# Performance work log

Measured on AMD Instinct MI355X. Metric: run time of the kernel, lower is better.

Reference implementation:

```python
import jax, jax.numpy as jnp
import numpy as np

B, S, DEC, ENC = 64, 4096, 512, 256


def setup_inputs() -> dict:
    key = jax.random.key(0)
    ks = jax.random.split(key, 8)
    scale_d = 1.0 / np.sqrt(DEC)
    scale_e = 1.0 / np.sqrt(ENC)
    return {
        "decoder_hidden": jax.random.normal(ks[0], (B, 1, DEC), jnp.float32),
        "encoder_outputs": jax.random.normal(ks[1], (B, S, ENC), jnp.float32),
        "mask": jax.random.randint(ks[2], (B, S), 0, 2, jnp.int32),
        "Wd": jax.random.normal(ks[3], (DEC, ENC), jnp.float32) * scale_d,
        "bd": jnp.zeros((ENC,), jnp.float32),
        "We": jax.random.normal(ks[4], (ENC, ENC), jnp.float32) * scale_e,
        "be": jnp.zeros((ENC,), jnp.float32),
        "Wa": jax.random.normal(ks[5], (ENC,), jnp.float32) * scale_e,
        "ba": jnp.zeros((1,), jnp.float32),
    }


def reference(decoder_hidden, encoder_outputs, mask, Wd, bd, We, be, Wa, ba):
    # decoder_proj: [B,1,ENC]; encoder_proj: [B,S,ENC]
    decoder_proj = jnp.einsum("bqd,de->bqe", decoder_hidden, Wd) + bd
    encoder_proj = jnp.einsum("bse,ef->bsf", encoder_outputs, We) + be
    energy = jnp.tanh(decoder_proj + encoder_proj)          # [B,S,ENC]
    scores = jnp.einsum("bse,e->bs", energy, Wa) + ba[0]     # [B,S]
    scores = jnp.where(mask == 0, jnp.float32(-1e10), scores)
    attn = jax.nn.softmax(scores, axis=1)                    # [B,S]
    context = jnp.einsum("bs,bse->be", attn, encoder_outputs)[:, None, :]  # [B,1,ENC]
    return context, attn
```

## Files before the change

### kernel.cpp

```cpp
#include <hip/hip_runtime.h>

#define BATCH 64
#define SEQ   4096
#define DECD  512
#define ENC   256
#define TS    128
#define NCHUNK (SEQ / TS)
#define OUT_ATTN (BATCH * ENC)

typedef short  short8  __attribute__((ext_vector_type(8)));
typedef float  floatx4 __attribute__((ext_vector_type(4)));

__device__ __forceinline__ short f2bf(float f) {
    union { float f; unsigned u; } v; v.f = f;
    unsigned u = v.u;
    u += 0x7FFFu + ((u >> 16) & 1u);
    return (short)(u >> 16);
}

__device__ __forceinline__ float bf2f(short s) {
    union { unsigned u; float f; } v;
    v.u = ((unsigned)(unsigned short)s) << 16;
    return v.f;
}

__device__ __forceinline__ float fast_tanh(float x) {
    x = fminf(fmaxf(x, -9.0f), 9.0f);
    float e2 = __expf(2.0f * x);
    float r  = __builtin_amdgcn_rcpf(e2 + 1.0f);
    return fmaf(-2.0f, r, 1.0f);
}

__device__ __forceinline__ void gload_lds16(const short* g, short* l) {
    __builtin_amdgcn_global_load_lds(
        (const __attribute__((address_space(1))) unsigned int*)g,
        (__attribute__((address_space(3))) unsigned int*)l,
        16, 0, 0);
}

__global__ void prep_kernel(const float* __restrict__ dh,
                            const float* __restrict__ Wd,
                            const float* __restrict__ bd,
                            const float* __restrict__ be,
                            const float* __restrict__ We,
                            float* __restrict__ dpb4,
                            short* __restrict__ WeF) {
    __shared__ float dhs[128];
    int blk = blockIdx.x;
    int t = threadIdx.x;
    if (blk < 256) {
        int b = blk >> 2, j = blk & 3;
        if (t < 128) dhs[t] = dh[b * DECD + j * 128 + t];
        __syncthreads();
        const float* wp = Wd + (size_t)(j * 128) * ENC + t;
        float a0 = 0.f, a1 = 0.f, a2 = 0.f, a3 = 0.f;
#pragma unroll 4
        for (int d = 0; d < 128; d += 4) {
            a0 = fmaf(dhs[d],     wp[(size_t)(d)     * ENC], a0);
            a1 = fmaf(dhs[d + 1], wp[(size_t)(d + 1) * ENC], a1);
            a2 = fmaf(dhs[d + 2], wp[(size_t)(d + 2) * ENC], a2);
            a3 = fmaf(dhs[d + 3], wp[(size_t)(d + 3) * ENC], a3);
        }
        float r = (a0 + a1) + (a2 + a3);
        if (j == 0) r += bd[t] + be[t];
        dpb4[(size_t)(b * 4 + j) * ENC + t] = r;
    } else {
        int gid  = (blk - 256) * 256 + t;
        int lane = gid & 63;
        int nt   = (gid >> 6) & 15;
        int kt   = gid >> 10;
        int quad = lane >> 4, l16 = lane & 15;
        int n = nt * 16 + l16;
        short8 v;
#pragma unroll
        for (int j = 0; j < 8; ++j) {
            int k = kt * 32 + quad * 8 + j;
            v[j] = f2bf(We[k * ENC + n]);
        }
        *(short8*)(WeF + gid * 8) = v;
    }
}

__global__ __launch_bounds__(512, 4) void main_kernel(
    const float* __restrict__ enc, const int* __restrict__ mask,
    const short* __restrict__ WeF, const float* __restrict__ dpb4,
    const float* __restrict__ Wa, const float* __restrict__ ba,
    float* __restrict__ out, float* __restrict__ ctx_ws, float* __restrict__ ml_ws)
{
    __shared__ short Bs[32768];
    float* F    = (float*)Bs;
    float* scF  = F;
    float* wgtF = F + 128;
    float* dpbF = F + 256;
    float* waF  = F + 512;
    float* ctxF = F + 768;

    int blk   = blockIdx.x;
    int b     = blk >> 5;
    int chunk = blk & 31;
    int s_base = chunk * TS;
    int t    = threadIdx.x;
    int w    = t >> 6, lane = t & 63;
    int quad = lane >> 4, l16 = lane & 15;

    const float* encB = enc + (size_t)b * SEQ * ENC;
    int row = s_base + w * 16 + l16;
    const float* aRow = encB + (size_t)row * ENC + quad * 8;

    short8 af[8];
#pragma unroll
    for (int kkt = 0; kkt < 4; ++kkt) {
        floatx4 q0 = *(const floatx4*)(aRow + kkt * 32);
        floatx4 q1 = *(const floatx4*)(aRow + kkt * 32 + 4);
        short8 a;
#pragma unroll
        for (int j = 0; j < 4; ++j) { a[j] = f2bf(q0[j]); a[j + 4] = f2bf(q1[j]); }
        af[kkt] = a;
    }

#pragma unroll
    for (int j = 0; j < 8; ++j) {
        int c = j * 8 + w;
        gload_lds16(WeF + c * 512 + lane * 8, Bs + c * 512 + lane * 8);
    }

#pragma unroll
    for (int kkt = 4; kkt < 8; ++kkt) {
        floatx4 q0 = *(const floatx4*)(aRow + kkt * 32);
        floatx4 q1 = *(const floatx4*)(aRow + kkt * 32 + 4);
        short8 a;
#pragma unroll
        for (int j = 0; j < 4; ++j) { a[j] = f2bf(q0[j]); a[j + 4] = f2bf(q1[j]); }
        af[kkt] = a;
    }

    floatx4 acc[16];
#pragma unroll
    for (int nt = 0; nt < 16; ++nt) acc[nt] = (floatx4){0.f, 0.f, 0.f, 0.f};

    __syncthreads();

#pragma unroll
    for (int kkt = 0; kkt < 4; ++kkt) {
        const short* bp = Bs + kkt * 8192 + lane * 8;
#pragma unroll
        for (int ng = 0; ng < 4; ++ng) {
            short8 bf0 = *(const short8*)(bp + (ng * 4 + 0) * 512);
            short8 bf1 = *(const short8*)(bp + (ng * 4 + 1) * 512);
            short8 bf2 = *(const short8*)(bp + (ng * 4 + 2) * 512);
            short8 bf3 = *(const short8*)(bp + (ng * 4 + 3) * 512);
            acc[ng * 4 + 0] = __builtin_amdgcn_mfma_f32_16x16x32_bf16(af[kkt], bf0, acc[ng * 4 + 0], 0, 0, 0);
            acc[ng * 4 + 1] = __builtin_amdgcn_mfma_f32_16x16x32_bf16(af[kkt], bf1, acc[ng * 4 + 1], 0, 0, 0);
            acc[ng * 4 + 2] = __builtin_amdgcn_mfma_f32_16x16x32_bf16(af[kkt], bf2, acc[ng * 4 + 2], 0, 0, 0);
            acc[ng * 4 + 3] = __builtin_amdgcn_mfma_f32_16x16x32_bf16(af[kkt], bf3, acc[ng * 4 + 3], 0, 0, 0);
        }
    }

    __syncthreads();
#pragma unroll
    for (int j = 0; j < 8; ++j) {
        int c = j * 8 + w;
        gload_lds16(WeF + 32768 + c * 512 + lane * 8, Bs + c * 512 + lane * 8);
    }
    __syncthreads();

#pragma unroll
    for (int kkt = 4; kkt < 8; ++kkt) {
        const short* bp = Bs + (kkt - 4) * 8192 + lane * 8;
#pragma unroll
        for (int ng = 0; ng < 4; ++ng) {
            short8 bf0 = *(const short8*)(bp + (ng * 4 + 0) * 512);
            short8 bf1 = *(const short8*)(bp + (ng * 4 + 1) * 512);
            short8 bf2 = *(const short8*)(bp + (ng * 4 + 2) * 512);
            short8 bf3 = *(const short8*)(bp + (ng * 4 + 3) * 512);
            acc[ng * 4 + 0] = __builtin_amdgcn_mfma_f32_16x16x32_bf16(af[kkt], bf0, acc[ng * 4 + 0], 0, 0, 0);
            acc[ng * 4 + 1] = __builtin_amdgcn_mfma_f32_16x16x32_bf16(af[kkt], bf1, acc[ng * 4 + 1], 0, 0, 0);
            acc[ng * 4 + 2] = __builtin_amdgcn_mfma_f32_16x16x32_bf16(af[kkt], bf2, acc[ng * 4 + 2], 0, 0, 0);
            acc[ng * 4 + 3] = __builtin_amdgcn_mfma_f32_16x16x32_bf16(af[kkt], bf3, acc[ng * 4 + 3], 0, 0, 0);
        }
    }

    __syncthreads();
    if (t < 256) {
        const float* dp = dpb4 + (size_t)b * 4 * ENC;
        dpbF[t] = dp[t] + dp[ENC + t] + dp[2 * ENC + t] + dp[3 * ENC + t];
    } else {
        waF[t - 256] = Wa[t - 256];
    }
    __syncthreads();

    float ba0 = ba[0];
    float part[4] = {0.f, 0.f, 0.f, 0.f};
#pragma unroll
    for (int nt = 0; nt < 16; ++nt) {
        int n = nt * 16 + l16;
        float wa  = waF[n];
        float dpv = dpbF[n];
#pragma unroll
        for (int r = 0; r < 4; ++r)
            part[r] = fmaf(wa, fast_tanh(acc[nt][r] + dpv), part[r]);
    }
#pragma unroll
    for (int r = 0; r < 4; ++r) {
        float v = part[r];
        v += __shfl_xor(v, 1);
        v += __shfl_xor(v, 2);
        v += __shfl_xor(v, 4);
        v += __shfl_xor(v, 8);
        part[r] = v;
    }
    if (l16 == 0) {
        int idx0 = w * 16 + quad * 4;
        int s0 = s_base + idx0;
        const int4 mv = *(const int4*)(mask + b * SEQ + s0);
        int mvals[4] = {mv.x, mv.y, mv.z, mv.w};
#pragma unroll
        for (int r = 0; r < 4; ++r) {
            float scv = part[r] + ba0;
            if (mvals[r] == 0) scv = -1e10f;
            scF[idx0 + r] = scv;
            out[OUT_ATTN + (size_t)b * SEQ + s0 + r] = scv;
        }
    }
    __syncthreads();

    float v0 = scF[lane], v1 = scF[lane + 64];
    float m = fmaxf(v0, v1);
    m = fmaxf(m, __shfl_xor(m, 1));
    m = fmaxf(m, __shfl_xor(m, 2));
    m = fmaxf(m, __shfl_xor(m, 4));
    m = fmaxf(m, __shfl_xor(m, 8));
    m = fmaxf(m, __shfl_xor(m, 16));
    m = fmaxf(m, __shfl_xor(m, 32));
    float e0 = __expf(v0 - m), e1 = __expf(v1 - m);
    float l = e0 + e1;
    l += __shfl_xor(l, 1);
    l += __shfl_xor(l, 2);
    l += __shfl_xor(l, 4);
    l += __shfl_xor(l, 8);
    l += __shfl_xor(l, 16);
    l += __shfl_xor(l, 32);
    if (t < TS) wgtF[t] = __expf(scF[t] - m);
    __syncthreads();

    float wrow = wgtF[w * 16 + l16];
#pragma unroll
    for (int kkt = 0; kkt < 8; ++kkt) {
        float c[8];
#pragma unroll
        for (int j = 0; j < 8; ++j)
            c[j] = wrow * bf2f(af[kkt][j]);
#pragma unroll
        for (int j = 0; j < 8; ++j) {
            c[j] += __shfl_xor(c[j], 1);
            c[j] += __shfl_xor(c[j], 2);
            c[j] += __shfl_xor(c[j], 4);
            c[j] += __shfl_xor(c[j], 8);
        }
        if (l16 == 0) {
            floatx4 u0 = {c[0], c[1], c[2], c[3]};
            floatx4 u1 = {c[4], c[5], c[6], c[7]};
            *(floatx4*)(ctxF + w * 256 + kkt * 32 + quad * 8)     = u0;
            *(floatx4*)(ctxF + w * 256 + kkt * 32 + quad * 8 + 4) = u1;
        }
    }
    __syncthreads();

    int cidx = b * NCHUNK + chunk;
    if (t < 256) {
        float cx = 0.f;
#pragma unroll
        for (int w2 = 0; w2 < 8; ++w2) cx += ctxF[w2 * 256 + t];
        ctx_ws[(size_t)cidx * ENC + t] = cx;
    }
    if (t == 0) {
        ml_ws[cidx * 2]     = m;
        ml_ws[cidx * 2 + 1] = l;
    }
}

__global__ void final_kernel(const float* __restrict__ ctx_ws,
                             const float* __restrict__ ml_ws,
                             float* __restrict__ out) {
    int blk = blockIdx.x, b = blk >> 3, j = blk & 7;
    int t = threadIdx.x;
    float m = -3.4e38f;
    for (int c = 0; c < NCHUNK; ++c)
        m = fmaxf(m, ml_ws[(b * NCHUNK + c) * 2]);
    float L = 0.f;
    for (int c = 0; c < NCHUNK; ++c)
        L += ml_ws[(b * NCHUNK + c) * 2 + 1] * __expf(ml_ws[(b * NCHUNK + c) * 2] - m);
    float inv = 1.0f / L;

    if (j == 0) {
        float cx = 0.f;
        for (int c = 0; c < NCHUNK; ++c) {
            float sc_c = __expf(ml_ws[(b * NCHUNK + c) * 2] - m);
            cx += sc_c * ctx_ws[(size_t)(b * NCHUNK + c) * ENC + t];
        }
        out[b * ENC + t] = cx * inv;
    }

    size_t base = OUT_ATTN + (size_t)b * SEQ + j * 512;
    float r0 = out[base + t];
    float r1 = out[base + 256 + t];
    out[base + t]       = __expf(r0 - m) * inv;
    out[base + 256 + t] = __expf(r1 - m) * inv;
}

extern "C" void kernel_launch(void* const* d_in, const int* in_sizes, int n_in,
                              void* d_out, int out_size, void* d_ws, size_t ws_size,
                              hipStream_t stream) {
    const float* dh   = (const float*)d_in[0];
    const float* enc  = (const float*)d_in[1];
    const int*   mask = (const int*)d_in[2];
    const float* Wd   = (const float*)d_in[3];
    const float* bd   = (const float*)d_in[4];
    const float* We   = (const float*)d_in[5];
    const float* be   = (const float*)d_in[6];
    const float* Wa   = (const float*)d_in[7];
    const float* ba   = (const float*)d_in[8];
    float* out = (float*)d_out;

    float* w      = (float*)d_ws;
    float* ctx_ws = w;
    float* ml_ws  = w + BATCH * NCHUNK * ENC;
    float* dpb4   = ml_ws + BATCH * NCHUNK * 2;
    short* WeF    = (short*)(dpb4 + BATCH * 4 * ENC);

    hipLaunchKernelGGL(prep_kernel,  dim3(256 + 32),       dim3(256), 0, stream,
                       dh, Wd, bd, be, We, dpb4, WeF);
    hipLaunchKernelGGL(main_kernel,  dim3(BATCH * NCHUNK), dim3(512), 0, stream,
                       enc, mask, WeF, dpb4, Wa, ba, out, ctx_ws, ml_ws);
    hipLaunchKernelGGL(final_kernel, dim3(BATCH * 8),      dim3(256), 0, stream,
                       ctx_ws, ml_ws, out);
}
```

Before: 491.7 us.

## Make main kernel persistent over eight chunks with We resident in LDS

```diff
diff --git a/kernel.cpp b/kernel.cpp
--- a/kernel.cpp
+++ b/kernel.cpp
@@ -6,6 +6,7 @@
 #define ENC   256
 #define TS    128
 #define NCHUNK (SEQ / TS)
+#define ITERS 8
 #define OUT_ATTN (BATCH * ENC)
 
 typedef short  short8  __attribute__((ext_vector_type(8)));
@@ -81,201 +82,184 @@
     }
 }
 
-__global__ __launch_bounds__(512, 4) void main_kernel(
+__global__ __launch_bounds__(512, 2) void main_kernel(
     const float* __restrict__ enc, const int* __restrict__ mask,
     const short* __restrict__ WeF, const float* __restrict__ dpb4,
     const float* __restrict__ Wa, const float* __restrict__ ba,
     float* __restrict__ out, float* __restrict__ ctx_ws, float* __restrict__ ml_ws)
 {
-    __shared__ short Bs[32768];
-    float* F    = (float*)Bs;
-    float* scF  = F;
-    float* wgtF = F + 128;
-    float* dpbF = F + 256;
-    float* waF  = F + 512;
-    float* ctxF = F + 768;
-
-    int blk   = blockIdx.x;
-    int b     = blk >> 5;
-    int chunk = blk & 31;
-    int s_base = chunk * TS;
+    __shared__ short Bs[65536];
+    __shared__ float scF[TS];
+    __shared__ float wgtF[TS];
+    __shared__ float dpbF[ENC];
+    __shared__ float waF[ENC];
+    __shared__ float ctxF[8 * ENC];
+
+    int blk    = blockIdx.x;
+    int b      = blk >> 2;
+    int chunk0 = (blk & 3) * ITERS;
     int t    = threadIdx.x;
     int w    = t >> 6, lane = t & 63;
     int quad = lane >> 4, l16 = lane & 15;
 
-    const float* encB = enc + (size_t)b * SEQ * ENC;
-    int row = s_base + w * 16 + l16;
-    const float* aRow = encB + (size_t)row * ENC + quad * 8;
-
-    short8 af[8];
-#pragma unroll
-    for (int kkt = 0; kkt < 4; ++kkt) {
-        floatx4 q0 = *(const floatx4*)(aRow + kkt * 32);
-        floatx4 q1 = *(const floatx4*)(aRow + kkt * 32 + 4);
-        short8 a;
-#pragma unroll
-        for (int j = 0; j < 4; ++j) { a[j] = f2bf(q0[j]); a[j + 4] = f2bf(q1[j]); }
-        af[kkt] = a;
-    }
-
-#pragma unroll
-    for (int j = 0; j < 8; ++j) {
-        int c = j * 8 + w;
-        gload_lds16(WeF + c * 512 + lane * 8, Bs + c * 512 + lane * 8);
-    }
-
-#pragma unroll
-    for (int kkt = 4; kkt < 8; ++kkt) {
-        floatx4 q0 = *(const floatx4*)(aRow + kkt * 32);
-        floatx4 q1 = *(const floatx4*)(aRow + kkt * 32 + 4);
-        short8 a;
-#pragma unroll
-        for (int j = 0; j < 4; ++j) { a[j] = f2bf(q0[j]); a[j + 4] = f2bf(q1[j]); }
-        af[kkt] = a;
-    }
-
-    floatx4 acc[16];
-#pragma unroll
-    for (int nt = 0; nt < 16; ++nt) acc[nt] = (floatx4){0.f, 0.f, 0.f, 0.f};
-
-    __syncthreads();
-
-#pragma unroll
-    for (int kkt = 0; kkt < 4; ++kkt) {
-        const short* bp = Bs + kkt * 8192 + lane * 8;
-#pragma unroll
-        for (int ng = 0; ng < 4; ++ng) {
-            short8 bf0 = *(const short8*)(bp + (ng * 4 + 0) * 512);
-            short8 bf1 = *(const short8*)(bp + (ng * 4 + 1) * 512);
-            short8 bf2 = *(const short8*)(bp + (ng * 4 + 2) * 512);
-            short8 bf3 = *(const short8*)(bp + (ng * 4 + 3) * 512);
-            acc[ng * 4 + 0] = __builtin_amdgcn_mfma_f32_16x16x32_bf16(af[kkt], bf0, acc[ng * 4 + 0], 0, 0, 0);
-            acc[ng * 4 + 1] = __builtin_amdgcn_mfma_f32_16x16x32_bf16(af[kkt], bf1, acc[ng * 4 + 1], 0, 0, 0);
-            acc[ng * 4 + 2] = __builtin_amdgcn_mfma_f32_16x16x32_bf16(af[kkt], bf2, acc[ng * 4 + 2], 0, 0, 0);
-            acc[ng * 4 + 3] = __builtin_amdgcn_mfma_f32_16x16x32_bf16(af[kkt], bf3, acc[ng * 4 + 3], 0, 0, 0);
-        }
-    }
-
-    __syncthreads();
-#pragma unroll
-    for (int j = 0; j < 8; ++j) {
-        int c = j * 8 + w;
-        gload_lds16(WeF + 32768 + c * 512 + lane * 8, Bs + c * 512 + lane * 8);
-    }
-    __syncthreads();
-
-#pragma unroll
-    for (int kkt = 4; kkt < 8; ++kkt) {
-        const short* bp = Bs + (kkt - 4) * 8192 + lane * 8;
-#pragma unroll
-        for (int ng = 0; ng < 4; ++ng) {
-            short8 bf0 = *(const short8*)(bp + (ng * 4 + 0) * 512);
-            short8 bf1 = *(const short8*)(bp + (ng * 4 + 1) * 512);
-            short8 bf2 = *(const short8*)(bp + (ng * 4 + 2) * 512);
-            short8 bf3 = *(const short8*)(bp + (ng * 4 + 3) * 512);
-            acc[ng * 4 + 0] = __builtin_amdgcn_mfma_f32_16x16x32_bf16(af[kkt], bf0, acc[ng * 4 + 0], 0, 0, 0);
-            acc[ng * 4 + 1] = __builtin_amdgcn_mfma_f32_16x16x32_bf16(af[kkt], bf1, acc[ng * 4 + 1], 0, 0, 0);
-            acc[ng * 4 + 2] = __builtin_amdgcn_mfma_f32_16x16x32_bf16(af[kkt], bf2, acc[ng * 4 + 2], 0, 0, 0);
-            acc[ng * 4 + 3] = __builtin_amdgcn_mfma_f32_16x16x32_bf16(af[kkt], bf3, acc[ng * 4 + 3], 0, 0, 0);
-        }
-    }
-
-    __syncthreads();
+    const float* encB  = enc + (size_t)b * SEQ * ENC;
+    const float* aRow0 = encB + (size_t)(chunk0 * TS + w * 16 + l16) * ENC + quad * 8;
+
+#pragma unroll
+    for (int j = 0; j < 16; ++j) {
+        int off = j * 4096 + w * 512 + lane * 8;
+        gload_lds16(WeF + off, Bs + off);
+    }
+
     if (t < 256) {
         const float* dp = dpb4 + (size_t)b * 4 * ENC;
         dpbF[t] = dp[t] + dp[ENC + t] + dp[2 * ENC + t] + dp[3 * ENC + t];
     } else {
         waF[t - 256] = Wa[t - 256];
     }
+    float ba0 = ba[0];
+
+    floatx4 pf[16];
+#pragma unroll
+    for (int q = 0; q < 8; ++q) {
+        pf[2 * q]     = *(const floatx4*)(aRow0 + q * 32);
+        pf[2 * q + 1] = *(const floatx4*)(aRow0 + q * 32 + 4);
+    }
+
     __syncthreads();
 
-    float ba0 = ba[0];
-    float part[4] = {0.f, 0.f, 0.f, 0.f};
-#pragma unroll
-    for (int nt = 0; nt < 16; ++nt) {
-        int n = nt * 16 + l16;
-        float wa  = waF[n];
-        float dpv = dpbF[n];
-#pragma unroll
-        for (int r = 0; r < 4; ++r)
-            part[r] = fmaf(wa, fast_tanh(acc[nt][r] + dpv), part[r]);
-    }
-#pragma unroll
-    for (int r = 0; r < 4; ++r) {
-        float v = part[r];
-        v += __shfl_xor(v, 1);
-        v += __shfl_xor(v, 2);
-        v += __shfl_xor(v, 4);
-        v += __shfl_xor(v, 8);
-        part[r] = v;
-    }
-    if (l16 == 0) {
-        int idx0 = w * 16 + quad * 4;
-        int s0 = s_base + idx0;
-        const int4 mv = *(const int4*)(mask + b * SEQ + s0);
-        int mvals[4] = {mv.x, mv.y, mv.z, mv.w};
+    for (int it = 0; it < ITERS; ++it) {
+        int chunk  = chunk0 + it;
+        int s_base = chunk * TS;
+
+        short8 af[8];
+#pragma unroll
+        for (int kkt = 0; kkt < 8; ++kkt) {
+            short8 a;
+#pragma unroll
+            for (int j = 0; j < 4; ++j) {
+                a[j]     = f2bf(pf[2 * kkt][j]);
+                a[j + 4] = f2bf(pf[2 * kkt + 1][j]);
+            }
+            af[kkt] = a;
+        }
+
+        if (it + 1 < ITERS) {
+            const float* aN = aRow0 + (size_t)(it + 1) * TS * ENC;
+#pragma unroll
+            for (int q = 0; q < 8; ++q) {
+                pf[2 * q]     = *(const floatx4*)(aN + q * 32);
+                pf[2 * q + 1] = *(const floatx4*)(aN + q * 32 + 4);
+            }
+        }
+
+        floatx4 acc[16];
+#pragma unroll
+        for (int nt = 0; nt < 16; ++nt) acc[nt] = (floatx4){0.f, 0.f, 0.f, 0.f};
+
+#pragma unroll
+        for (int kkt = 0; kkt < 8; ++kkt) {
+            const short* bp = Bs + kkt * 8192 + lane * 8;
+#pragma unroll
+            for (int ng = 0; ng < 4; ++ng) {
+                short8 bf0 = *(const short8*)(bp + (ng * 4 + 0) * 512);
+                short8 bf1 = *(const short8*)(bp + (ng * 4 + 1) * 512);
+                short8 bf2 = *(const short8*)(bp + (ng * 4 + 2) * 512);
+                short8 bf3 = *(const short8*)(bp + (ng * 4 + 3) * 512);
+                acc[ng * 4 + 0] = __builtin_amdgcn_mfma_f32_16x16x32_bf16(af[kkt], bf0, acc[ng * 4 + 0], 0, 0, 0);
+                acc[ng * 4 + 1] = __builtin_amdgcn_mfma_f32_16x16x32_bf16(af[kkt], bf1, acc[ng * 4 + 1], 0, 0, 0);
+                acc[ng * 4 + 2] = __builtin_amdgcn_mfma_f32_16x16x32_bf16(af[kkt], bf2, acc[ng * 4 + 2], 0, 0, 0);
+                acc[ng * 4 + 3] = __builtin_amdgcn_mfma_f32_16x16x32_bf16(af[kkt], bf3, acc[ng * 4 + 3], 0, 0, 0);
+            }
+        }
+
+        float part[4] = {0.f, 0.f, 0.f, 0.f};
+#pragma unroll
+        for (int nt = 0; nt < 16; ++nt) {
+            int n = nt * 16 + l16;
+            float wa  = waF[n];
+            float dpv = dpbF[n];
+#pragma unroll
+            for (int r = 0; r < 4; ++r)
+                part[r] = fmaf(wa, fast_tanh(acc[nt][r] + dpv), part[r]);
+        }
 #pragma unroll
         for (int r = 0; r < 4; ++r) {
-            float scv = part[r] + ba0;
-            if (mvals[r] == 0) scv = -1e10f;
-            scF[idx0 + r] = scv;
-            out[OUT_ATTN + (size_t)b * SEQ + s0 + r] = scv;
-        }
-    }
-    __syncthreads();
-
-    float v0 = scF[lane], v1 = scF[lane + 64];
-    float m = fmaxf(v0, v1);
-    m = fmaxf(m, __shfl_xor(m, 1));
-    m = fmaxf(m, __shfl_xor(m, 2));
-    m = fmaxf(m, __shfl_xor(m, 4));
-    m = fmaxf(m, __shfl_xor(m, 8));
-    m = fmaxf(m, __shfl_xor(m, 16));
-    m = fmaxf(m, __shfl_xor(m, 32));
-    float e0 = __expf(v0 - m), e1 = __expf(v1 - m);
-    float l = e0 + e1;
-    l += __shfl_xor(l, 1);
-    l += __shfl_xor(l, 2);
-    l += __shfl_xor(l, 4);
-    l += __shfl_xor(l, 8);
-    l += __shfl_xor(l, 16);
-    l += __shfl_xor(l, 32);
-    if (t < TS) wgtF[t] = __expf(scF[t] - m);
-    __syncthreads();
-
-    float wrow = wgtF[w * 16 + l16];
-#pragma unroll
-    for (int kkt = 0; kkt < 8; ++kkt) {
-        float c[8];
-#pragma unroll
-        for (int j = 0; j < 8; ++j)
-            c[j] = wrow * bf2f(af[kkt][j]);
-#pragma unroll
-        for (int j = 0; j < 8; ++j) {
-            c[j] += __shfl_xor(c[j], 1);
-            c[j] += __shfl_xor(c[j], 2);
-            c[j] += __shfl_xor(c[j], 4);
-            c[j] += __shfl_xor(c[j], 8);
+            float v = part[r];
+            v += __shfl_xor(v, 1);
+            v += __shfl_xor(v, 2);
+            v += __shfl_xor(v, 4);
+            v += __shfl_xor(v, 8);
+            part[r] = v;
         }
         if (l16 == 0) {
-            floatx4 u0 = {c[0], c[1], c[2], c[3]};
-            floatx4 u1 = {c[4], c[5], c[6], c[7]};
-            *(floatx4*)(ctxF + w * 256 + kkt * 32 + quad * 8)     = u0;
-            *(floatx4*)(ctxF + w * 256 + kkt * 32 + quad * 8 + 4) = u1;
-        }
-    }
-    __syncthreads();
-
-    int cidx = b * NCHUNK + chunk;
-    if (t < 256) {
-        float cx = 0.f;
-#pragma unroll
-        for (int w2 = 0; w2 < 8; ++w2) cx += ctxF[w2 * 256 + t];
-        ctx_ws[(size_t)cidx * ENC + t] = cx;
-    }
-    if (t == 0) {
-        ml_ws[cidx * 2]     = m;
-        ml_ws[cidx * 2 + 1] = l;
+            int idx0 = w * 16 + quad * 4;
+            int s0 = s_base + idx0;
+            const int4 mv = *(const int4*)(mask + b * SEQ + s0);
+            int mvals[4] = {mv.x, mv.y, mv.z, mv.w};
+#pragma unroll
+            for (int r = 0; r < 4; ++r) {
+                float scv = part[r] + ba0;
+                if (mvals[r] == 0) scv = -1e10f;
+                scF[idx0 + r] = scv;
+                out[OUT_ATTN + (size_t)b * SEQ + s0 + r] = scv;
+            }
+        }
+        __syncthreads();
+
+        float v0 = scF[lane], v1 = scF[lane + 64];
+        float m = fmaxf(v0, v1);
+        m = fmaxf(m, __shfl_xor(m, 1));
+        m = fmaxf(m, __shfl_xor(m, 2));
+        m = fmaxf(m, __shfl_xor(m, 4));
+        m = fmaxf(m, __shfl_xor(m, 8));
+        m = fmaxf(m, __shfl_xor(m, 16));
+        m = fmaxf(m, __shfl_xor(m, 32));
+        float e0 = __expf(v0 - m), e1 = __expf(v1 - m);
+        float l = e0 + e1;
+        l += __shfl_xor(l, 1);
+        l += __shfl_xor(l, 2);
+        l += __shfl_xor(l, 4);
+        l += __shfl_xor(l, 8);
+        l += __shfl_xor(l, 16);
+        l += __shfl_xor(l, 32);
+        if (t < TS) wgtF[t] = __expf(scF[t] - m);
+        __syncthreads();
+
+        float wrow = wgtF[w * 16 + l16];
+#pragma unroll
+        for (int kkt = 0; kkt < 8; ++kkt) {
+            float c[8];
+#pragma unroll
+            for (int j = 0; j < 8; ++j)
+                c[j] = wrow * bf2f(af[kkt][j]);
+#pragma unroll
+            for (int j = 0; j < 8; ++j) {
+                c[j] += __shfl_xor(c[j], 1);
+                c[j] += __shfl_xor(c[j], 2);
+                c[j] += __shfl_xor(c[j], 4);
+                c[j] += __shfl_xor(c[j], 8);
+            }
+            if (l16 == 0) {
+                floatx4 u0 = {c[0], c[1], c[2], c[3]};
+                floatx4 u1 = {c[4], c[5], c[6], c[7]};
+                *(floatx4*)(ctxF + w * 256 + kkt * 32 + quad * 8)     = u0;
+                *(floatx4*)(ctxF + w * 256 + kkt * 32 + quad * 8 + 4) = u1;
+            }
+        }
+        __syncthreads();
+
+        int cidx = b * NCHUNK + chunk;
+        if (t < 256) {
+            float cx = 0.f;
+#pragma unroll
+            for (int w2 = 0; w2 < 8; ++w2) cx += ctxF[w2 * 256 + t];
+            ctx_ws[(size_t)cidx * ENC + t] = cx;
+        }
+        if (t == 0) {
+            ml_ws[cidx * 2]     = m;
+            ml_ws[cidx * 2 + 1] = l;
+        }
     }
 }
 
@@ -324,14 +308,15 @@
 
     float* w      = (float*)d_ws;
     float* ctx_ws = w;
-    float* ml_ws  = w + BATCH * NCHUNK * ENC;
+    float* ml_ws  = w + BATCH * NCHUNK * 2 * ENC;
+    ml_ws  = w + BATCH * NCHUNK * ENC;
     float* dpb4   = ml_ws + BATCH * NCHUNK * 2;
     short* WeF    = (short*)(dpb4 + BATCH * 4 * ENC);
 
-    hipLaunchKernelGGL(prep_kernel,  dim3(256 + 32),       dim3(256), 0, stream,
+    hipLaunchKernelGGL(prep_kernel,  dim3(256 + 32), dim3(256), 0, stream,
                        dh, Wd, bd, be, We, dpb4, WeF);
-    hipLaunchKernelGGL(main_kernel,  dim3(BATCH * NCHUNK), dim3(512), 0, stream,
+    hipLaunchKernelGGL(main_kernel,  dim3(256),      dim3(512), 0, stream,
                        enc, mask, WeF, dpb4, Wa, ba, out, ctx_ws, ml_ws);
-    hipLaunchKernelGGL(final_kernel, dim3(BATCH * 8),      dim3(256), 0, stream,
+    hipLaunchKernelGGL(final_kernel, dim3(BATCH * 8), dim3(256), 0, stream,
                        ctx_ws, ml_ws, out);
 }
```

New measurement: 430.7 us. 1.14x faster.
